# Kernel tuning notes

Hardware: AMD Instinct MI355X
Metric: run time of the kernel (lower is better)

Reference implementation:

```python
import jax, jax.numpy as jnp
import numpy as np

N, E, IN_DIM, H, D, EDGE_DIM, T = 50000, 800000, 128, 4, 32, 32, 8
NEG_SLOPE = 0.2


def setup_inputs() -> dict:
    key = jax.random.key(0)
    ks = jax.random.split(key, 12)
    s = 0.1  # xavier-ish scale
    return {
        "h": jax.random.normal(ks[0], (N, IN_DIM), jnp.float32),
        "W": jax.random.normal(ks[1], (IN_DIM, D * H), jnp.float32) * s,
        "edge_emb": jax.random.normal(ks[2], (T, EDGE_DIM), jnp.float32) * s,
        "W_r": jax.random.normal(ks[3], (T, EDGE_DIM, EDGE_DIM * H), jnp.float32) * s,
        "a_l": jax.random.normal(ks[4], (1, H, D), jnp.float32) * s,
        "a_r": jax.random.normal(ks[5], (1, H, D), jnp.float32) * s,
        "a_e": jax.random.normal(ks[6], (1, H, EDGE_DIM), jnp.float32) * s,
        "res_w": jax.random.normal(ks[7], (IN_DIM, D * H), jnp.float32) * s,
        "res_b": jnp.zeros((D * H,), jnp.float32),
        "row": jax.random.randint(ks[8], (E,), 0, N),  # src node per edge
        "col": jax.random.randint(ks[9], (E,), 0, N),  # dst node per edge
        "etype": jax.random.randint(ks[10], (E,), 0, T),
    }


def reference(h, W, edge_emb, W_r, a_l, a_r, a_e, res_w, res_b, row, col, etype):
    # node projection: [N, H, D]
    emb = (h @ W).reshape(-1, H, D)

    # TypedLinear on edge-type embeddings. Since edge features depend only on
    # etype, compute the per-type result once, then gather per edge.
    e_t = jnp.einsum('te,tef->tf', edge_emb, W_r).reshape(T, H, EDGE_DIM)
    h_e_t = (a_e * e_t).sum(-1)            # [T, H]

    h_l = (a_l * emb).sum(-1)              # [N, H]
    h_r = (a_r * emb).sum(-1)              # [N, H]
    scores = h_l[row] + h_r[col] + h_e_t[etype]          # [E, H]
    scores = jax.nn.leaky_relu(scores, NEG_SLOPE)

    # segment softmax over edges sharing the same destination node (col)
    m = jax.ops.segment_max(scores, col, num_segments=N)  # [N, H]
    ex = jnp.exp(scores - m[col])
    denom = jax.ops.segment_sum(ex, col, num_segments=N)
    alpha = ex / denom[col]                # [E, H]

    # u_mul_e + scatter-sum to destination nodes
    msg = emb[row] * alpha[:, :, None]     # [E, H, D]
    agg = jax.ops.segment_sum(msg, col, num_segments=N)   # [N, H, D]

    # original permutes to [N, D, H] before flattening (d-major layout)
    out = jnp.transpose(agg, (0, 2, 1)).reshape(-1, D * H)
    out = out + h @ res_w + res_b          # residual
    return jax.nn.elu(out)
```

## Files before the change

kernel.cpp:

```cpp
#include <hip/hip_runtime.h>
#include <math.h>

#define NH 4
#define EDIM 32
#define NEG_SLOPE 0.2f
#define BSH 5
#define BCAP 1024

typedef __attribute__((ext_vector_type(8))) short short8;
typedef __attribute__((ext_vector_type(4))) float f32x4;
typedef __attribute__((ext_vector_type(2))) float f32x2;

__device__ __forceinline__ unsigned short f2bf(float f) {
    unsigned int x = __builtin_bit_cast(unsigned int, f);
    unsigned int r = (x + 0x7fffu + ((x >> 16) & 1u)) >> 16;
    return (unsigned short)r;
}
__device__ __forceinline__ float bf2f(unsigned short u) {
    unsigned int x = ((unsigned int)u) << 16;
    return __builtin_bit_cast(float, x);
}

__global__ __launch_bounds__(256) void k_prep(
    const float* __restrict__ W, const float* __restrict__ Rw,
    unsigned short* __restrict__ Wt, unsigned short* __restrict__ Rwt,
    int* __restrict__ bucket_cursor,
    const float* __restrict__ edge_emb, const float* __restrict__ W_r,
    const float* __restrict__ a_e, float* __restrict__ h_e_t)
{
    int tid = threadIdx.x;
    if (blockIdx.x < 64) {
        int idx = blockIdx.x * 256 + tid;
        int n = idx >> 7, k = idx & 127;
        Wt[n * 128 + k]  = f2bf(W[k * 128 + n]);
        Rwt[n * 128 + k] = f2bf(Rw[k * 128 + n]);
        if (idx < 2048) bucket_cursor[idx] = 0;
        return;
    }
    int t = blockIdx.x - 64;
    if (tid < 128) {
        int rem = tid;
        float v = 0.f;
#pragma unroll
        for (int e = 0; e < EDIM; ++e)
            v += edge_emb[t * EDIM + e] * W_r[(size_t)(t * EDIM + e) * 128 + rem];
        v *= a_e[rem];
#pragma unroll
        for (int off = 16; off >= 1; off >>= 1)
            v += __shfl_xor(v, off);
        if ((rem & 31) == 0) h_e_t[t * NH + (rem >> 5)] = v;
    }
}

__global__ __launch_bounds__(256) void k_gemm_fill(
    const float* __restrict__ A, const unsigned short* __restrict__ Wt,
    const unsigned short* __restrict__ Rwt, const float* __restrict__ Rb,
    const float* __restrict__ a_l, const float* __restrict__ a_r,
    unsigned short* __restrict__ EmbBf, unsigned short* __restrict__ ResBf,
    float* __restrict__ h_l, float* __restrict__ h_r, int M,
    const int* __restrict__ row, const int* __restrict__ col,
    const int* __restrict__ etype, int* __restrict__ bucket_cursor,
    unsigned* __restrict__ ebuf, int E, int NB, int nFill)
{
    __shared__ char lds[32768];
    int tid = threadIdx.x;

    if ((int)blockIdx.x < nFill) {
        int* bins = (int*)lds;
        int* base = bins + 2048;
        for (int i = tid; i < NB; i += 256) bins[i] = 0;
        __syncthreads();
        int lo = blockIdx.x * 8192;
        int ccol[32];
#pragma unroll
        for (int u = 0; u < 32; ++u) {
            int i = lo + tid + u * 256;
            int c = (i < E) ? col[i] : -1;
            ccol[u] = c;
            if (c >= 0) atomicAdd(&bins[c >> BSH], 1);
        }
        __syncthreads();
        for (int i = tid; i < NB; i += 256) {
            int c = bins[i];
            base[i] = c ? atomicAdd(&bucket_cursor[i], c) : 0;
            bins[i] = 0;
        }
        __syncthreads();
#pragma unroll
        for (int u = 0; u < 32; ++u) {
            int i = lo + tid + u * 256;
            int c = ccol[u];
            if (c >= 0) {
                int bk = c >> BSH;
                int p = bk * BCAP + base[bk] + atomicAdd(&bins[bk], 1);
                ebuf[p] = (unsigned)row[i] | ((unsigned)etype[i] << 16)
                        | ((unsigned)(c & 31) << 24);
            }
        }
        return;
    }

    int m0 = ((int)blockIdx.x - nFill) * 64;
#pragma unroll
    for (int i = 0; i < 4; ++i) {
        int c = tid + 256 * i;
        int r = c >> 4, kc = c & 15;
        int grow = m0 + r;
        float4 v0 = make_float4(0.f, 0.f, 0.f, 0.f), v1 = v0;
        if (grow < M) {
            v0 = *(const float4*)&A[(size_t)grow * 128 + kc * 8];
            v1 = *(const float4*)&A[(size_t)grow * 128 + kc * 8 + 4];
        }
        union { unsigned short u[8]; uint4 v; } p;
        p.u[0] = f2bf(v0.x); p.u[1] = f2bf(v0.y); p.u[2] = f2bf(v0.z); p.u[3] = f2bf(v0.w);
        p.u[4] = f2bf(v1.x); p.u[5] = f2bf(v1.y); p.u[6] = f2bf(v1.z); p.u[7] = f2bf(v1.w);
        int b = (r * 256 + kc * 16) ^ ((r & 7) << 4);
        *(uint4*)&lds[b] = p.v;
    }

    int w = tid >> 6, lane = tid & 63;
    int g = lane >> 4, l15 = lane & 15;
    int lrow = w * 16 + l15;

    auto stageB = [&](const unsigned short* src) {
#pragma unroll
        for (int i = 0; i < 4; ++i) {
            int c = tid + 256 * i;
            int n2 = c >> 4, kc = c & 15;
            uint4 v = *(const uint4*)&src[n2 * 128 + kc * 8];
            int b = 16384 + ((n2 * 256 + kc * 16) ^ ((n2 & 7) << 4));
            *(uint4*)&lds[b] = v;
        }
    };
    auto computeHalf = [&](f32x4* accp, const short8* a) {
#pragma unroll
        for (int f = 0; f < 4; ++f) {
            int n2 = f * 16 + l15;
            int nsw = (n2 & 7) << 4;
#pragma unroll
            for (int s = 0; s < 4; ++s) {
                short8 b = *(const short8*)&lds[16384 + ((n2 * 256 + s * 64 + g * 16) ^ nsw)];
                accp[f] = __builtin_amdgcn_mfma_f32_16x16x32_bf16(a[s], b, accp[f], 0, 0, 0);
            }
        }
    };

    stageB(Wt);
    __syncthreads();

    short8 a[4];
#pragma unroll
    for (int s = 0; s < 4; ++s)
        a[s] = *(const short8*)&lds[(lrow * 256 + s * 64 + g * 16) ^ ((lrow & 7) << 4)];

    f32x4 acc[8];
#pragma unroll
    for (int f = 0; f < 8; ++f) acc[f] = (f32x4){0.f, 0.f, 0.f, 0.f};

    computeHalf(&acc[0], a);
    __syncthreads();
    stageB(Wt + 64 * 128);
    __syncthreads();
    computeHalf(&acc[4], a);

#pragma unroll
    for (int f = 0; f < 8; ++f) {
        int col2 = f * 16 + l15;
#pragma unroll
        for (int reg = 0; reg < 4; ++reg) {
            int grow = m0 + w * 16 + g * 4 + reg;
            if (grow < M) EmbBf[(size_t)grow * 128 + col2] = f2bf(acc[f][reg]);
        }
    }
    {
        float alv[8], arv[8];
#pragma unroll
        for (int f = 0; f < 8; ++f) {
            alv[f] = a_l[f * 16 + l15];
            arv[f] = a_r[f * 16 + l15];
        }
#pragma unroll
        for (int reg = 0; reg < 4; ++reg) {
            float4 hl4, hr4;
#pragma unroll
            for (int hh = 0; hh < 4; ++hh) {
                float pl = alv[2 * hh] * acc[2 * hh][reg] + alv[2 * hh + 1] * acc[2 * hh + 1][reg];
                float pr = arv[2 * hh] * acc[2 * hh][reg] + arv[2 * hh + 1] * acc[2 * hh + 1][reg];
#pragma unroll
                for (int off = 8; off >= 1; off >>= 1) {
                    pl += __shfl_xor(pl, off);
                    pr += __shfl_xor(pr, off);
                }
                (&hl4.x)[hh] = pl;
                (&hr4.x)[hh] = pr;
            }
            int grow = m0 + w * 16 + g * 4 + reg;
            if (l15 == 0 && grow < M) {
                *(float4*)&h_l[(size_t)grow * 4] = hl4;
                *(float4*)&h_r[(size_t)grow * 4] = hr4;
            }
        }
    }

    __syncthreads();
    stageB(Rwt);
    __syncthreads();
#pragma unroll
    for (int f = 0; f < 8; ++f) acc[f] = (f32x4){0.f, 0.f, 0.f, 0.f};
    computeHalf(&acc[0], a);
    __syncthreads();
    stageB(Rwt + 64 * 128);
    __syncthreads();
    computeHalf(&acc[4], a);

#pragma unroll
    for (int f = 0; f < 8; ++f) {
        int col2 = f * 16 + l15;
        float bias = Rb[col2];
#pragma unroll
        for (int reg = 0; reg < 4; ++reg) {
            int grow = m0 + w * 16 + g * 4 + reg;
            if (grow < M) ResBf[(size_t)grow * 128 + col2] = f2bf(acc[f][reg] + bias);
        }
    }
}

__global__ __launch_bounds__(512) void k_sort_aggregate(
    const unsigned* __restrict__ ebuf, const int* __restrict__ bucket_cursor,
    const float* __restrict__ h_l, const float* __restrict__ h_e_t,
    const float* __restrict__ h_r, const unsigned short* __restrict__ embBf,
    const unsigned short* __restrict__ resBf, float* __restrict__ out, int N)
{
    __shared__ int sedge[BCAP];
    __shared__ int cnt[32];
    __shared__ int scn[33];
    __shared__ char shalpha[8 * 1536];

    int b = blockIdx.x;
    int tid = threadIdx.x;
    int seg = b * BCAP;
    int m = bucket_cursor[b];

    if (tid < 32) cnt[tid] = 0;
    __syncthreads();
    for (int i = tid; i < m; i += 512)
        atomicAdd(&cnt[(ebuf[seg + i] >> 24) & 31], 1);
    __syncthreads();
    if (tid < 32) {
        int v = cnt[tid];
        int s = v;
#pragma unroll
        for (int off = 1; off < 32; off <<= 1) {
            int u2 = __shfl_up(s, off);
            if (tid >= off) s += u2;
        }
        scn[tid + 1] = s;
        if (tid == 0) scn[0] = 0;
        cnt[tid] = s - v;
    }
    __syncthreads();
    for (int i = tid; i < m; i += 512) {
        unsigned e = ebuf[seg + i];
        int p = atomicAdd(&cnt[(e >> 24) & 31], 1);
        sedge[p] = (int)(e & 0x00FFFFFFu);
    }
    __syncthreads();

    int w = tid >> 6, lane = tid & 63;
    int myh = lane >> 4;
    int l31 = lane & 31;
    int sel = lane >> 5;
    int hq = l31 >> 3;
    int loff = l31 * 8;
    char* wb = &shalpha[w * 1536];
    const char* ab2 = wb + 256 + hq * 260;
    const char* embByte = (const char*)embBf;

    for (int it = 0; it < 4; ++it) {
        int nd = it * 8 + w;
        int n = b * 32 + nd;
        if (n >= N) break;
        int st0 = scn[nd];
        int deg = scn[nd + 1] - st0;
        float4 hrv = *(const float4*)&h_r[(size_t)n * 4];

        if (deg <= 64) {
            bool act = lane < deg;
            float p0 = 0.f, p1 = 0.f, p2 = 0.f, p3 = 0.f;
            int roval = 0;
            if (act) {
                int pk = sedge[st0 + lane];
                roval = (pk & 0xffff) << 8;
                float4 hl = *(const float4*)&h_l[(size_t)(pk & 0xffff) * 4];
                float4 he = *(const float4*)&h_e_t[(size_t)(pk >> 16) * 4];
                float sc0 = hl.x + he.x + hrv.x; sc0 = sc0 > 0.f ? sc0 : NEG_SLOPE * sc0;
                float sc1 = hl.y + he.y + hrv.y; sc1 = sc1 > 0.f ? sc1 : NEG_SLOPE * sc1;
                float sc2 = hl.z + he.z + hrv.z; sc2 = sc2 > 0.f ? sc2 : NEG_SLOPE * sc2;
                float sc3 = hl.w + he.w + hrv.w; sc3 = sc3 > 0.f ? sc3 : NEG_SLOPE * sc3;
                p0 = __expf(sc0); p1 = __expf(sc1);
                p2 = __expf(sc2); p3 = __expf(sc3);
            }
            *(int*)(wb + lane * 4) = roval;
            *(float*)(wb + 256 + 0 * 260 + lane * 4) = p0;
            *(float*)(wb + 256 + 1 * 260 + lane * 4) = p1;
            *(float*)(wb + 256 + 2 * 260 + lane * 4) = p2;
            *(float*)(wb + 256 + 3 * 260 + lane * 4) = p3;

            float d0 = p0, d1 = p1, d2 = p2, d3 = p3;
#pragma unroll
            for (int off = 32; off >= 1; off >>= 1) {
                d0 += __shfl_xor(d0, off); d1 += __shfl_xor(d1, off);
                d2 += __shfl_xor(d2, off); d3 += __shfl_xor(d3, off);
            }
            float den = hq == 0 ? d0 : hq == 1 ? d1 : hq == 2 ? d2 : d3;
            float inv = (deg > 0) ? __builtin_amdgcn_rcpf(den) : 0.f;

            f32x4 acc4 = (f32x4){0.f, 0.f, 0.f, 0.f};
            for (int q = 0; q < deg; q += 8) {
                int ro[4]; float aq[4];
#pragma unroll
                for (int u = 0; u < 4; ++u) {
                    int qe = q + 2 * u + sel;
                    ro[u] = *(const int*)(wb + qe * 4);
                    aq[u] = *(const float*)(ab2 + qe * 4);
                }
                uint2 ev[4];
#pragma unroll
                for (int u = 0; u < 4; ++u)
                    ev[u] = *(const uint2*)(embByte + (size_t)(unsigned)(ro[u] + loff));
#pragma unroll
                for (int u = 0; u < 4; ++u) {
                    f32x4 ef;
                    ef.x = __builtin_bit_cast(float, ev[u].x << 16);
                    ef.y = __builtin_bit_cast(float, ev[u].x & 0xffff0000u);
                    ef.z = __builtin_bit_cast(float, ev[u].y << 16);
                    ef.w = __builtin_bit_cast(float, ev[u].y & 0xffff0000u);
                    acc4 = __builtin_elementwise_fma(
                        ef, (f32x4){aq[u], aq[u], aq[u], aq[u]}, acc4);
                }
            }
            acc4.x += __shfl_xor(acc4.x, 32);
            acc4.y += __shfl_xor(acc4.y, 32);
            acc4.z += __shfl_xor(acc4.z, 32);
            acc4.w += __shfl_xor(acc4.w, 32);
            float vlo = sel ? acc4.z : acc4.x;
            float vhi = sel ? acc4.w : acc4.y;

            int j0 = l31 * 4 + sel * 2;
            int h0 = j0 >> 5, dd = j0 & 31;
            size_t ob = (size_t)n * 128;
            float o0 = vlo * inv + bf2f(resBf[ob + dd * 4 + h0]);
            float o1 = vhi * inv + bf2f(resBf[ob + (dd + 1) * 4 + h0]);
            out[ob + dd * 4 + h0] = o0 > 0.f ? o0 : expm1f(o0);
            out[ob + (dd + 1) * 4 + h0] = o1 > 0.f ? o1 : expm1f(o1);
        } else {
            f32x2 acc2 = (f32x2){0.f, 0.f};
            float d0 = 0.f, d1 = 0.f, d2 = 0.f, d3 = 0.f;
            for (int base2 = 0; base2 < deg; base2 += 64) {
                int el = base2 + lane;
                if (el < deg) {
                    int pk = sedge[st0 + el];
                    float4 hl = *(const float4*)&h_l[(size_t)(pk & 0xffff) * 4];
                    float4 he = *(const float4*)&h_e_t[(size_t)(pk >> 16) * 4];
                    float sc0 = hl.x + he.x + hrv.x; sc0 = sc0 > 0.f ? sc0 : NEG_SLOPE * sc0;
                    float sc1 = hl.y + he.y + hrv.y; sc1 = sc1 > 0.f ? sc1 : NEG_SLOPE * sc1;
                    float sc2 = hl.z + he.z + hrv.z; sc2 = sc2 > 0.f ? sc2 : NEG_SLOPE * sc2;
                    float sc3 = hl.w + he.w + hrv.w; sc3 = sc3 > 0.f ? sc3 : NEG_SLOPE * sc3;
                    d0 += __expf(sc0); d1 += __expf(sc1);
                    d2 += __expf(sc2); d3 += __expf(sc3);
                }
            }
#pragma unroll
            for (int off = 32; off >= 1; off >>= 1) {
                d0 += __shfl_xor(d0, off); d1 += __shfl_xor(d1, off);
                d2 += __shfl_xor(d2, off); d3 += __shfl_xor(d3, off);
            }
            float den = myh == 0 ? d0 : myh == 1 ? d1 : myh == 2 ? d2 : d3;
            float inv = __builtin_amdgcn_rcpf(den);
            for (int base2 = 0; base2 < deg; base2 += 64) {
                int el = base2 + lane;
                float p0 = 0.f, p1 = 0.f, p2 = 0.f, p3 = 0.f;
                int r = 0;
                if (el < deg) {
                    int pk = sedge[st0 + el];
                    r = pk & 0xffff;
                    float4 hl = *(const float4*)&h_l[(size_t)r * 4];
                    float4 he = *(const float4*)&h_e_t[(size_t)(pk >> 16) * 4];
                    float sc0 = hl.x + he.x + hrv.x; sc0 = sc0 > 0.f ? sc0 : NEG_SLOPE * sc0;
                    float sc1 = hl.y + he.y + hrv.y; sc1 = sc1 > 0.f ? sc1 : NEG_SLOPE * sc1;
                    float sc2 = hl.z + he.z + hrv.z; sc2 = sc2 > 0.f ? sc2 : NEG_SLOPE * sc2;
                    float sc3 = hl.w + he.w + hrv.w; sc3 = sc3 > 0.f ? sc3 : NEG_SLOPE * sc3;
                    p0 = __expf(sc0); p1 = __expf(sc1);
                    p2 = __expf(sc2); p3 = __expf(sc3);
                }
                int cmax = (deg - base2 < 64) ? (deg - base2) : 64;
                for (int qq = 0; qq < cmax; ++qq) {
                    int rq = __shfl(r, qq);
                    float a0 = __shfl(p0, qq), a1 = __shfl(p1, qq);
                    float a2 = __shfl(p2, qq), a3 = __shfl(p3, qq);
                    float aqv = myh == 0 ? a0 : myh == 1 ? a1 : myh == 2 ? a2 : a3;
                    unsigned int ev = *(const unsigned int*)&embBf[(size_t)rq * 128 + lane * 2];
                    f32x2 ef;
                    ef.x = __builtin_bit_cast(float, ev << 16);
                    ef.y = __builtin_bit_cast(float, ev & 0xffff0000u);
                    acc2 = __builtin_elementwise_fma(ef, (f32x2){aqv, aqv}, acc2);
                }
            }
            int j0 = lane * 2;
            int h0 = j0 >> 5, dd0 = j0 & 31;
            size_t ob = (size_t)n * 128;
            float o0 = acc2.x * inv + bf2f(resBf[ob + dd0 * 4 + h0]);
            float o1 = acc2.y * inv + bf2f(resBf[ob + (dd0 + 1) * 4 + h0]);
            out[ob + dd0 * 4 + h0] = o0 > 0.f ? o0 : expm1f(o0);
            out[ob + (dd0 + 1) * 4 + h0] = o1 > 0.f ? o1 : expm1f(o1);
        }
    }
}

extern "C" void kernel_launch(void* const* d_in, const int* in_sizes, int n_in,
                              void* d_out, int out_size, void* d_ws, size_t ws_size,
                              hipStream_t stream)
{
    const float* h        = (const float*)d_in[0];
    const float* W        = (const float*)d_in[1];
    const float* edge_emb = (const float*)d_in[2];
    const float* W_r      = (const float*)d_in[3];
    const float* a_l      = (const float*)d_in[4];
    const float* a_r      = (const float*)d_in[5];
    const float* a_e      = (const float*)d_in[6];
    const float* res_w    = (const float*)d_in[7];
    const float* res_b    = (const float*)d_in[8];
    const int*   row      = (const int*)d_in[9];
    const int*   col      = (const int*)d_in[10];
    const int*   etype    = (const int*)d_in[11];
    float* out = (float*)d_out;

    int N = in_sizes[0] / 128;
    int E = in_sizes[9];
    int T = in_sizes[2] / EDIM;
    int NB = (N + 31) >> BSH;

    char* ws = (char*)d_ws;
    size_t off = 0;
    auto alloc = [&](size_t bytes) -> char* {
        char* p = ws + off;
        off = (off + bytes + 255) & ~(size_t)255;
        return p;
    };
    unsigned short* embBf = (unsigned short*)alloc((size_t)N * 128 * 2);
    unsigned short* resBf = (unsigned short*)alloc((size_t)N * 128 * 2);
    unsigned short* Wt    = (unsigned short*)alloc((size_t)128 * 128 * 2);
    unsigned short* Rwt   = (unsigned short*)alloc((size_t)128 * 128 * 2);
    float* h_l   = (float*)alloc((size_t)N * 4 * 4);
    float* h_r   = (float*)alloc((size_t)N * 4 * 4);
    float* h_e_t = (float*)alloc((size_t)T * NH * 4);
    int* bucket_cursor = (int*)alloc(2048 * 4);
    unsigned* ebuf = (unsigned*)alloc((size_t)(NB + 1) * BCAP * 4);

    int nFill = (E + 8191) / 8192;
    int nGemm = (N + 63) / 64;

    hipLaunchKernelGGL(k_prep, dim3(64 + T), dim3(256), 0, stream,
                       W, res_w, Wt, Rwt, bucket_cursor,
                       edge_emb, W_r, a_e, h_e_t);
    hipLaunchKernelGGL(k_gemm_fill, dim3(nFill + nGemm), dim3(256), 0, stream,
                       h, Wt, Rwt, res_b, a_l, a_r, embBf, resBf, h_l, h_r, N,
                       row, col, etype, bucket_cursor, ebuf, E, NB, nFill);
    hipLaunchKernelGGL(k_sort_aggregate, dim3(NB), dim3(512), 0, stream,
                       ebuf, bucket_cursor, h_l, h_e_t, h_r, embBf, resBf, out, N);
}
```

Before: 81.80 us.

## Process two destination nodes per wavefront when both have degree at most 32

Each wavefront now takes a pair of destination nodes. When both have degree ≤32, each half-wave (32 lanes) handles one node, scoring its edges and accumulating all 8 column chunks per iteration without the cross-half shuffle reduction. The previous one-node-per-wave path is kept as a fallback for pairs with larger degrees. With average degree around 16, most pairs take the new path, which is meant to cut idle lanes and loop overhead for low-degree nodes. The cost is more divergent control flow, larger register arrays (8 gathers in flight), and iterations set by the larger degree of the pair.

```diff
diff --git a/kernel.cpp b/kernel.cpp
--- a/kernel.cpp
+++ b/kernel.cpp
@@ -262,7 +262,7 @@
     for (int i = tid; i < m; i += 512) {
         unsigned e = ebuf[seg + i];
         int p = atomicAdd(&cnt[(e >> 24) & 31], 1);
-        sedge[p] = (int)(e & 0x00FFFFFFu);
+        sedge[p] = (int)(e & 0x00FFFFFF);
     }
     __syncthreads();
 
@@ -276,20 +276,24 @@
     const char* ab2 = wb + 256 + hq * 260;
     const char* embByte = (const char*)embBf;
 
-    for (int it = 0; it < 4; ++it) {
-        int nd = it * 8 + w;
-        int n = b * 32 + nd;
-        if (n >= N) break;
-        int st0 = scn[nd];
-        int deg = scn[nd + 1] - st0;
-        float4 hrv = *(const float4*)&h_r[(size_t)n * 4];
-
-        if (deg <= 64) {
-            bool act = lane < deg;
+    for (int it = 0; it < 2; ++it) {
+        int ndA = it * 16 + w * 2;
+        int degA = scn[ndA + 1] - scn[ndA];
+        int degB = scn[ndA + 2] - scn[ndA + 1];
+
+        if (degA <= 32 && degB <= 32) {
+            int nd = ndA + sel;
+            int n = b * 32 + nd;
+            bool okn = (n < N);
+            int st0 = scn[nd];
+            int deg = scn[nd + 1] - st0;
+            int nsafe = okn ? n : 0;
+            float4 hrv = *(const float4*)&h_r[(size_t)nsafe * 4];
+            bool act = okn && (l31 < deg);
             float p0 = 0.f, p1 = 0.f, p2 = 0.f, p3 = 0.f;
             int roval = 0;
             if (act) {
-                int pk = sedge[st0 + lane];
+                int pk = sedge[st0 + l31];
                 roval = (pk & 0xffff) << 8;
                 float4 hl = *(const float4*)&h_l[(size_t)(pk & 0xffff) * 4];
                 float4 he = *(const float4*)&h_e_t[(size_t)(pk >> 16) * 4];
@@ -308,28 +312,30 @@
 
             float d0 = p0, d1 = p1, d2 = p2, d3 = p3;
 #pragma unroll
-            for (int off = 32; off >= 1; off >>= 1) {
+            for (int off = 16; off >= 1; off >>= 1) {
                 d0 += __shfl_xor(d0, off); d1 += __shfl_xor(d1, off);
                 d2 += __shfl_xor(d2, off); d3 += __shfl_xor(d3, off);
             }
             float den = hq == 0 ? d0 : hq == 1 ? d1 : hq == 2 ? d2 : d3;
             float inv = (deg > 0) ? __builtin_amdgcn_rcpf(den) : 0.f;
 
+            int degmax = degA > degB ? degA : degB;
+            int sb = lane & 32;
             f32x4 acc4 = (f32x4){0.f, 0.f, 0.f, 0.f};
-            for (int q = 0; q < deg; q += 8) {
-                int ro[4]; float aq[4];
-#pragma unroll
-                for (int u = 0; u < 4; ++u) {
-                    int qe = q + 2 * u + sel;
-                    ro[u] = *(const int*)(wb + qe * 4);
-                    aq[u] = *(const float*)(ab2 + qe * 4);
-                }
-                uint2 ev[4];
-#pragma unroll
-                for (int u = 0; u < 4; ++u)
+            for (int q = 0; q < degmax; q += 8) {
+                int ro[8]; float aq[8];
+#pragma unroll
+                for (int u = 0; u < 8; ++u) {
+                    int slot = sb + q + u;
+                    ro[u] = *(const int*)(wb + slot * 4);
+                    aq[u] = *(const float*)(ab2 + slot * 4);
+                }
+                uint2 ev[8];
+#pragma unroll
+                for (int u = 0; u < 8; ++u)
                     ev[u] = *(const uint2*)(embByte + (size_t)(unsigned)(ro[u] + loff));
 #pragma unroll
-                for (int u = 0; u < 4; ++u) {
+                for (int u = 0; u < 8; ++u) {
                     f32x4 ef;
                     ef.x = __builtin_bit_cast(float, ev[u].x << 16);
                     ef.y = __builtin_bit_cast(float, ev[u].x & 0xffff0000u);
@@ -339,52 +345,35 @@
                         ef, (f32x4){aq[u], aq[u], aq[u], aq[u]}, acc4);
                 }
             }
-            acc4.x += __shfl_xor(acc4.x, 32);
-            acc4.y += __shfl_xor(acc4.y, 32);
-            acc4.z += __shfl_xor(acc4.z, 32);
-            acc4.w += __shfl_xor(acc4.w, 32);
-            float vlo = sel ? acc4.z : acc4.x;
-            float vhi = sel ? acc4.w : acc4.y;
-
-            int j0 = l31 * 4 + sel * 2;
-            int h0 = j0 >> 5, dd = j0 & 31;
-            size_t ob = (size_t)n * 128;
-            float o0 = vlo * inv + bf2f(resBf[ob + dd * 4 + h0]);
-            float o1 = vhi * inv + bf2f(resBf[ob + (dd + 1) * 4 + h0]);
-            out[ob + dd * 4 + h0] = o0 > 0.f ? o0 : expm1f(o0);
-            out[ob + (dd + 1) * 4 + h0] = o1 > 0.f ? o1 : expm1f(o1);
-        } else {
-            f32x2 acc2 = (f32x2){0.f, 0.f};
-            float d0 = 0.f, d1 = 0.f, d2 = 0.f, d3 = 0.f;
-            for (int base2 = 0; base2 < deg; base2 += 64) {
-                int el = base2 + lane;
-                if (el < deg) {
-                    int pk = sedge[st0 + el];
+            if (okn) {
+                int h0 = hq;
+                int ddb = (l31 & 7) * 4;
+                size_t ob = (size_t)n * 128;
+#pragma unroll
+                for (int u = 0; u < 4; ++u) {
+                    float o = acc4[u] * inv + bf2f(resBf[ob + (ddb + u) * 4 + h0]);
+                    out[ob + (ddb + u) * 4 + h0] = o > 0.f ? o : expm1f(o);
+                }
+            }
+            continue;
+        }
+
+        for (int pick = 0; pick < 2; ++pick) {
+            int nd = ndA + pick;
+            int n = b * 32 + nd;
+            if (n >= N) continue;
+            int st0 = scn[nd];
+            int deg = scn[nd + 1] - st0;
+            float4 hrv = *(const float4*)&h_r[(size_t)n * 4];
+
+            if (deg <= 64) {
+                bool act = lane < deg;
+                float p0 = 0.f, p1 = 0.f, p2 = 0.f, p3 = 0.f;
+                int roval = 0;
+                if (act) {
+                    int pk = sedge[st0 + lane];
+                    roval = (pk & 0xffff) << 8;
                     float4 hl = *(const float4*)&h_l[(size_t)(pk & 0xffff) * 4];
-                    float4 he = *(const float4*)&h_e_t[(size_t)(pk >> 16) * 4];
-                    float sc0 = hl.x + he.x + hrv.x; sc0 = sc0 > 0.f ? sc0 : NEG_SLOPE * sc0;
-                    float sc1 = hl.y + he.y + hrv.y; sc1 = sc1 > 0.f ? sc1 : NEG_SLOPE * sc1;
-                    float sc2 = hl.z + he.z + hrv.z; sc2 = sc2 > 0.f ? sc2 : NEG_SLOPE * sc2;
-                    float sc3 = hl.w + he.w + hrv.w; sc3 = sc3 > 0.f ? sc3 : NEG_SLOPE * sc3;
-                    d0 += __expf(sc0); d1 += __expf(sc1);
-                    d2 += __expf(sc2); d3 += __expf(sc3);
-                }
-            }
-#pragma unroll
-            for (int off = 32; off >= 1; off >>= 1) {
-                d0 += __shfl_xor(d0, off); d1 += __shfl_xor(d1, off);
-                d2 += __shfl_xor(d2, off); d3 += __shfl_xor(d3, off);
-            }
-            float den = myh == 0 ? d0 : myh == 1 ? d1 : myh == 2 ? d2 : d3;
-            float inv = __builtin_amdgcn_rcpf(den);
-            for (int base2 = 0; base2 < deg; base2 += 64) {
-                int el = base2 + lane;
-                float p0 = 0.f, p1 = 0.f, p2 = 0.f, p3 = 0.f;
-                int r = 0;
-                if (el < deg) {
-                    int pk = sedge[st0 + el];
-                    r = pk & 0xffff;
-                    float4 hl = *(const float4*)&h_l[(size_t)r * 4];
                     float4 he = *(const float4*)&h_e_t[(size_t)(pk >> 16) * 4];
                     float sc0 = hl.x + he.x + hrv.x; sc0 = sc0 > 0.f ? sc0 : NEG_SLOPE * sc0;
                     float sc1 = hl.y + he.y + hrv.y; sc1 = sc1 > 0.f ? sc1 : NEG_SLOPE * sc1;
@@ -393,26 +382,120 @@
                     p0 = __expf(sc0); p1 = __expf(sc1);
                     p2 = __expf(sc2); p3 = __expf(sc3);
                 }
-                int cmax = (deg - base2 < 64) ? (deg - base2) : 64;
-                for (int qq = 0; qq < cmax; ++qq) {
-                    int rq = __shfl(r, qq);
-                    float a0 = __shfl(p0, qq), a1 = __shfl(p1, qq);
-                    float a2 = __shfl(p2, qq), a3 = __shfl(p3, qq);
-                    float aqv = myh == 0 ? a0 : myh == 1 ? a1 : myh == 2 ? a2 : a3;
-                    unsigned int ev = *(const unsigned int*)&embBf[(size_t)rq * 128 + lane * 2];
-                    f32x2 ef;
-                    ef.x = __builtin_bit_cast(float, ev << 16);
-                    ef.y = __builtin_bit_cast(float, ev & 0xffff0000u);
-                    acc2 = __builtin_elementwise_fma(ef, (f32x2){aqv, aqv}, acc2);
-                }
-            }
-            int j0 = lane * 2;
-            int h0 = j0 >> 5, dd0 = j0 & 31;
-            size_t ob = (size_t)n * 128;
-            float o0 = acc2.x * inv + bf2f(resBf[ob + dd0 * 4 + h0]);
-            float o1 = acc2.y * inv + bf2f(resBf[ob + (dd0 + 1) * 4 + h0]);
-            out[ob + dd0 * 4 + h0] = o0 > 0.f ? o0 : expm1f(o0);
-            out[ob + (dd0 + 1) * 4 + h0] = o1 > 0.f ? o1 : expm1f(o1);
+                *(int*)(wb + lane * 4) = roval;
+                *(float*)(wb + 256 + 0 * 260 + lane * 4) = p0;
+                *(float*)(wb + 256 + 1 * 260 + lane * 4) = p1;
+                *(float*)(wb + 256 + 2 * 260 + lane * 4) = p2;
+                *(float*)(wb + 256 + 3 * 260 + lane * 4) = p3;
+
+                float d0 = p0, d1 = p1, d2 = p2, d3 = p3;
+#pragma unroll
+                for (int off = 32; off >= 1; off >>= 1) {
+                    d0 += __shfl_xor(d0, off); d1 += __shfl_xor(d1, off);
+                    d2 += __shfl_xor(d2, off); d3 += __shfl_xor(d3, off);
+                }
+                float den = hq == 0 ? d0 : hq == 1 ? d1 : hq == 2 ? d2 : d3;
+                float inv = (deg > 0) ? __builtin_amdgcn_rcpf(den) : 0.f;
+
+                f32x4 acc4 = (f32x4){0.f, 0.f, 0.f, 0.f};
+                for (int q = 0; q < deg; q += 8) {
+                    int ro[4]; float aq[4];
+#pragma unroll
+                    for (int u = 0; u < 4; ++u) {
+                        int qe = q + 2 * u + sel;
+                        ro[u] = *(const int*)(wb + qe * 4);
+                        aq[u] = *(const float*)(ab2 + qe * 4);
+                    }
+                    uint2 ev[4];
+#pragma unroll
+                    for (int u = 0; u < 4; ++u)
+                        ev[u] = *(const uint2*)(embByte + (size_t)(unsigned)(ro[u] + loff));
+#pragma unroll
+                    for (int u = 0; u < 4; ++u) {
+                        f32x4 ef;
+                        ef.x = __builtin_bit_cast(float, ev[u].x << 16);
+                        ef.y = __builtin_bit_cast(float, ev[u].x & 0xffff0000u);
+                        ef.z = __builtin_bit_cast(float, ev[u].y << 16);
+                        ef.w = __builtin_bit_cast(float, ev[u].y & 0xffff0000u);
+                        acc4 = __builtin_elementwise_fma(
+                            ef, (f32x4){aq[u], aq[u], aq[u], aq[u]}, acc4);
+                    }
+                }
+                acc4.x += __shfl_xor(acc4.x, 32);
+                acc4.y += __shfl_xor(acc4.y, 32);
+                acc4.z += __shfl_xor(acc4.z, 32);
+                acc4.w += __shfl_xor(acc4.w, 32);
+                float vlo = sel ? acc4.z : acc4.x;
+                float vhi = sel ? acc4.w : acc4.y;
+
+                int j0 = l31 * 4 + sel * 2;
+                int h0 = j0 >> 5, dd = j0 & 31;
+                size_t ob = (size_t)n * 128;
+                float o0 = vlo * inv + bf2f(resBf[ob + dd * 4 + h0]);
+                float o1 = vhi * inv + bf2f(resBf[ob + (dd + 1) * 4 + h0]);
+                out[ob + dd * 4 + h0] = o0 > 0.f ? o0 : expm1f(o0);
+                out[ob + (dd + 1) * 4 + h0] = o1 > 0.f ? o1 : expm1f(o1);
+            } else {
+                f32x2 acc2 = (f32x2){0.f, 0.f};
+                float d0 = 0.f, d1 = 0.f, d2 = 0.f, d3 = 0.f;
+                for (int base2 = 0; base2 < deg; base2 += 64) {
+                    int el = base2 + lane;
+                    if (el < deg) {
+                        int pk = sedge[st0 + el];
+                        float4 hl = *(const float4*)&h_l[(size_t)(pk & 0xffff) * 4];
+                        float4 he = *(const float4*)&h_e_t[(size_t)(pk >> 16) * 4];
+                        float sc0 = hl.x + he.x + hrv.x; sc0 = sc0 > 0.f ? sc0 : NEG_SLOPE * sc0;
+                        float sc1 = hl.y + he.y + hrv.y; sc1 = sc1 > 0.f ? sc1 : NEG_SLOPE * sc1;
+                        float sc2 = hl.z + he.z + hrv.z; sc2 = sc2 > 0.f ? sc2 : NEG_SLOPE * sc2;
+                        float sc3 = hl.w + he.w + hrv.w; sc3 = sc3 > 0.f ? sc3 : NEG_SLOPE * sc3;
+                        d0 += __expf(sc0); d1 += __expf(sc1);
+                        d2 += __expf(sc2); d3 += __expf(sc3);
+                    }
+                }
+#pragma unroll
+                for (int off = 32; off >= 1; off >>= 1) {
+                    d0 += __shfl_xor(d0, off); d1 += __shfl_xor(d1, off);
+                    d2 += __shfl_xor(d2, off); d3 += __shfl_xor(d3, off);
+                }
+                float den = myh == 0 ? d0 : myh == 1 ? d1 : myh == 2 ? d2 : d3;
+                float inv = __builtin_amdgcn_rcpf(den);
+                for (int base2 = 0; base2 < deg; base2 += 64) {
+                    int el = base2 + lane;
+                    float p0 = 0.f, p1 = 0.f, p2 = 0.f, p3 = 0.f;
+                    int r = 0;
+                    if (el < deg) {
+                        int pk = sedge[st0 + el];
+                        r = pk & 0xffff;
+                        float4 hl = *(const float4*)&h_l[(size_t)r * 4];
+                        float4 he = *(const float4*)&h_e_t[(size_t)(pk >> 16) * 4];
+                        float sc0 = hl.x + he.x + hrv.x; sc0 = sc0 > 0.f ? sc0 : NEG_SLOPE * sc0;
+                        float sc1 = hl.y + he.y + hrv.y; sc1 = sc1 > 0.f ? sc1 : NEG_SLOPE * sc1;
+                        float sc2 = hl.z + he.z + hrv.z; sc2 = sc2 > 0.f ? sc2 : NEG_SLOPE * sc2;
+                        float sc3 = hl.w + he.w + hrv.w; sc3 = sc3 > 0.f ? sc3 : NEG_SLOPE * sc3;
+                        p0 = __expf(sc0); p1 = __expf(sc1);
+                        p2 = __expf(sc2); p3 = __expf(sc3);
+                    }
+                    int cmax = (deg - base2 < 64) ? (deg - base2) : 64;
+                    for (int qq = 0; qq < cmax; ++qq) {
+                        int rq = __shfl(r, qq);
+                        float a0 = __shfl(p0, qq), a1 = __shfl(p1, qq);
+                        float a2 = __shfl(p2, qq), a3 = __shfl(p3, qq);
+                        float aqv = myh == 0 ? a0 : myh == 1 ? a1 : myh == 2 ? a2 : a3;
+                        unsigned int ev = *(const unsigned int*)&embBf[(size_t)rq * 128 + lane * 2];
+                        f32x2 ef;
+                        ef.x = __builtin_bit_cast(float, ev << 16);
+                        ef.y = __builtin_bit_cast(float, ev & 0xffff0000u);
+                        acc2 = __builtin_elementwise_fma(ef, (f32x2){aqv, aqv}, acc2);
+                    }
+                }
+                int j0 = lane * 2;
+                int h0 = j0 >> 5, dd0 = j0 & 31;
+                size_t ob = (size_t)n * 128;
+                float o0 = acc2.x * inv + bf2f(resBf[ob + dd0 * 4 + h0]);
+                float o1 = acc2.y * inv + bf2f(resBf[ob + (dd0 + 1) * 4 + h0]);
+                out[ob + dd0 * 4 + h0] = o0 > 0.f ? o0 : expm1f(o0);
+                out[ob + (dd0 + 1) * 4 + h0] = o1 > 0.f ? o1 : expm1f(o1);
+            }
         }
     }
 }
```

New measurement: 86.56 us. 1.06x slower.
